# Optimization experiments

Hardware: AMD Instinct MI355X
Metric: run time of the kernel (lower is better)

Reference implementation:

```python
import jax, jax.numpy as jnp
import numpy as np

TIME_SHIFT_START = 256
VELOCITY_START = 768
NOTE_OFF_START = 128
RHYTHM_W = 1.0
HARMONY_W = 1.0
MELODY_W = 1.0


def setup_inputs() -> dict:
    key = jax.random.key(0)
    tokens = jax.random.randint(key, (512, 16384), 0, 774, dtype=jnp.int64)
    return {"tokens": tokens}


def reference(tokens) -> jnp.ndarray:
    batch_size, seq_len = tokens.shape

    # --- rhythm consistency: |diff| of time-shift indicator, mean over all ---
    time_shifts = ((tokens >= TIME_SHIFT_START) & (tokens < VELOCITY_START)).astype(jnp.float32)
    rhythm_loss = jnp.abs(jnp.diff(time_shifts, axis=1)).mean()

    # --- harmonic coherence: vectorized version of the per-position loop ---
    # original: sum_i mean_b(harsh[:, i]) / seq_len  ==  harsh.sum() / (batch * seq_len)
    note_on_mask = tokens < NOTE_OFF_START
    pitches = tokens * note_on_mask.astype(tokens.dtype)
    pitch_classes = pitches % 12                      # [B, S]
    interval = jnp.abs(pitch_classes[:, :-1] - pitch_classes[:, 1:])  # [B, S-1]
    harsh = ((interval == 6) | (interval == 11)).astype(jnp.float32)
    harmony_loss = harsh.sum() / (batch_size * seq_len)

    # --- melodic smoothness: large leap (>12 semitones) rate ---
    pitch_diffs = jnp.diff(pitches.astype(jnp.float32), axis=1)
    melody_loss = (jnp.abs(pitch_diffs) > 12).astype(jnp.float32).mean()

    return RHYTHM_W * rhythm_loss + HARMONY_W * harmony_loss + MELODY_W * melody_loss
```

## Files before the change

### kernel.cpp

```cpp
#include <hip/hip_runtime.h>

constexpr int B = 512;
constexpr int S = 16384;
constexpr int NTOK = B * S;
constexpr int TPT = 32;
constexpr int NBLOCKS = NTOK / TPT / 256;

__global__ __launch_bounds__(256) void mpl_main(const int* __restrict__ tokens,
                                                unsigned int* __restrict__ partials) {
    const int tid = blockIdx.x * 256 + threadIdx.x;
    const int lane = threadIdx.x & 63;
    const int t0 = tid * TPT;

    int toks[TPT + 1];
    const int4* p = reinterpret_cast<const int4*>(tokens + t0);
#pragma unroll
    for (int v = 0; v < TPT / 4; ++v) {
        int4 x = p[v];
        toks[v * 4 + 0] = x.x;
        toks[v * 4 + 1] = x.y;
        toks[v * 4 + 2] = x.z;
        toks[v * 4 + 3] = x.w;
    }

    int nxt = __shfl(toks[0], lane + 1, 64);
    if (lane == 63) {
        const bool rowEnd = ((t0 + TPT) & (S - 1)) == 0;
        nxt = rowEnd ? toks[TPT - 1] : tokens[t0 + TPT];
    }
    toks[TPT] = nxt;

    int rc = 0, hc = 0, mc = 0;
    int qp = 0, pcp = 0, pitp = 0;
#pragma unroll
    for (int j = 0; j <= TPT; ++j) {
        const int t = toks[j];
        const int q = (t + 256) >> 9;
        const int pit = (t < 128) ? t : 0;
        const int pc = pit % 12;
        if (j > 0) {
            rc += (qp ^ q) & 1;
            const int xh = pcp - pc + 11;
            hc += (0x00420021u >> xh) & 1;
            const unsigned ym = (unsigned)(pitp - pit + 12);
            mc += (ym > 24u) ? 1 : 0;
        }
        qp = q; pcp = pc; pitp = pit;
    }

    unsigned int pk = (unsigned)rc | ((unsigned)mc << 16);
    unsigned int hh = (unsigned)hc;
#pragma unroll
    for (int off = 32; off > 0; off >>= 1) {
        pk += __shfl_down(pk, off, 64);
        hh += __shfl_down(hh, off, 64);
    }

    __shared__ unsigned int s[2][4];
    const int wave = threadIdx.x >> 6;
    if ((threadIdx.x & 63) == 0) {
        s[0][wave] = pk;
        s[1][wave] = hh;
    }
    __syncthreads();
    if (threadIdx.x == 0) {
        partials[blockIdx.x]           = s[0][0] + s[0][1] + s[0][2] + s[0][3];
        partials[NBLOCKS + blockIdx.x] = s[1][0] + s[1][1] + s[1][2] + s[1][3];
    }
}

__global__ __launch_bounds__(256) void mpl_reduce(const unsigned int* __restrict__ partials,
                                                  float* __restrict__ out) {
    const uint4* ppk = reinterpret_cast<const uint4*>(partials);
    const uint4* phh = reinterpret_cast<const uint4*>(partials + NBLOCKS);
    unsigned int r = 0, m = 0, h = 0;
#pragma unroll 1
    for (int j = threadIdx.x; j < NBLOCKS / 4; j += 256) {
        uint4 a = ppk[j];
        r += (a.x & 0xFFFFu) + (a.y & 0xFFFFu) + (a.z & 0xFFFFu) + (a.w & 0xFFFFu);
        m += (a.x >> 16) + (a.y >> 16) + (a.z >> 16) + (a.w >> 16);
        uint4 b = phh[j];
        h += b.x + b.y + b.z + b.w;
    }
#pragma unroll
    for (int off = 32; off > 0; off >>= 1) {
        r += __shfl_down(r, off, 64);
        m += __shfl_down(m, off, 64);
        h += __shfl_down(h, off, 64);
    }
    __shared__ unsigned int s[3][4];
    const int wave = threadIdx.x >> 6;
    if ((threadIdx.x & 63) == 0) {
        s[0][wave] = r; s[1][wave] = m; s[2][wave] = h;
    }
    __syncthreads();
    if (threadIdx.x == 0) {
        unsigned int rt = s[0][0] + s[0][1] + s[0][2] + s[0][3];
        unsigned int mt = s[1][0] + s[1][1] + s[1][2] + s[1][3];
        unsigned int ht = s[2][0] + s[2][1] + s[2][2] + s[2][3];
        const double pairs = (double)B * (double)(S - 1);
        const double all = (double)B * (double)S;
        out[0] = (float)((double)rt / pairs + (double)ht / all + (double)mt / pairs);
    }
}

extern "C" void kernel_launch(void* const* d_in, const int* in_sizes, int n_in,
                              void* d_out, int out_size, void* d_ws, size_t ws_size,
                              hipStream_t stream) {
    const int* tokens = (const int*)d_in[0];
    unsigned int* partials = (unsigned int*)d_ws;

    mpl_main<<<NBLOCKS, 256, 0, stream>>>(tokens, partials);
    mpl_reduce<<<1, 256, 0, stream>>>(partials, (float*)d_out);
}
```

Baseline: 15.83 us.

## Fuse final reduction into main kernel via atomics and last-block ticket

Drops the separate reduce kernel launch. Each block atomically adds a packed 64-bit value holding its rhythm, harmony and melody counts into one of 32 cache-line-spaced accumulators, then takes a ticket. The last block sums the accumulators and writes the output. This needs a memset of the workspace before each call, so one launch is replaced by a memset plus atomic traffic, and the 21-bit packed fields rely on carry handling.

```diff
diff --git a/kernel.cpp b/kernel.cpp
--- a/kernel.cpp
+++ b/kernel.cpp
@@ -5,9 +5,12 @@
 constexpr int NTOK = B * S;
 constexpr int TPT = 32;
 constexpr int NBLOCKS = NTOK / TPT / 256;
+constexpr int NLINES = 32;
+constexpr int WS_ZERO_BYTES = NLINES * 64 + 64;
 
-__global__ __launch_bounds__(256) void mpl_main(const int* __restrict__ tokens,
-                                                unsigned int* __restrict__ partials) {
+__global__ __launch_bounds__(256) void mpl_fused(const int* __restrict__ tokens,
+                                                 unsigned long long* __restrict__ ws64,
+                                                 float* __restrict__ out) {
     const int tid = blockIdx.x * 256 + threadIdx.x;
     const int lane = threadIdx.x & 63;
     const int t0 = tid * TPT;
@@ -57,50 +60,50 @@
     }
 
     __shared__ unsigned int s[2][4];
+    __shared__ unsigned int sLast;
     const int wave = threadIdx.x >> 6;
     if ((threadIdx.x & 63) == 0) {
         s[0][wave] = pk;
         s[1][wave] = hh;
     }
     __syncthreads();
+
+    unsigned int* ticket = reinterpret_cast<unsigned int*>(ws64 + NLINES * 8);
+
     if (threadIdx.x == 0) {
-        partials[blockIdx.x]           = s[0][0] + s[0][1] + s[0][2] + s[0][3];
-        partials[NBLOCKS + blockIdx.x] = s[1][0] + s[1][1] + s[1][2] + s[1][3];
-    }
-}
-
-__global__ __launch_bounds__(256) void mpl_reduce(const unsigned int* __restrict__ partials,
-                                                  float* __restrict__ out) {
-    const uint4* ppk = reinterpret_cast<const uint4*>(partials);
-    const uint4* phh = reinterpret_cast<const uint4*>(partials + NBLOCKS);
-    unsigned int r = 0, m = 0, h = 0;
-#pragma unroll 1
-    for (int j = threadIdx.x; j < NBLOCKS / 4; j += 256) {
-        uint4 a = ppk[j];
-        r += (a.x & 0xFFFFu) + (a.y & 0xFFFFu) + (a.z & 0xFFFFu) + (a.w & 0xFFFFu);
-        m += (a.x >> 16) + (a.y >> 16) + (a.z >> 16) + (a.w >> 16);
-        uint4 b = phh[j];
-        h += b.x + b.y + b.z + b.w;
-    }
-#pragma unroll
-    for (int off = 32; off > 0; off >>= 1) {
-        r += __shfl_down(r, off, 64);
-        m += __shfl_down(m, off, 64);
-        h += __shfl_down(h, off, 64);
-    }
-    __shared__ unsigned int s[3][4];
-    const int wave = threadIdx.x >> 6;
-    if ((threadIdx.x & 63) == 0) {
-        s[0][wave] = r; s[1][wave] = m; s[2][wave] = h;
+        const unsigned int pks = s[0][0] + s[0][1] + s[0][2] + s[0][3];
+        const unsigned int hs  = s[1][0] + s[1][1] + s[1][2] + s[1][3];
+        const unsigned long long packed =
+            (unsigned long long)(pks & 0xFFFFu) |
+            ((unsigned long long)hs << 21) |
+            ((unsigned long long)(pks >> 16) << 42);
+        const int line = (blockIdx.x & (NLINES - 1)) * 8;
+        unsigned long long prev = atomicAdd(&ws64[line], packed);
+        unsigned int bump = (unsigned int)(prev >> 63);
+        unsigned int old = atomicAdd(ticket, 1u + bump);
+        sLast = (old == (unsigned)(NBLOCKS - 1)) ? 1u : 0u;
     }
     __syncthreads();
-    if (threadIdx.x == 0) {
-        unsigned int rt = s[0][0] + s[0][1] + s[0][2] + s[0][3];
-        unsigned int mt = s[1][0] + s[1][1] + s[1][2] + s[1][3];
-        unsigned int ht = s[2][0] + s[2][1] + s[2][2] + s[2][3];
-        const double pairs = (double)B * (double)(S - 1);
-        const double all = (double)B * (double)S;
-        out[0] = (float)((double)rt / pairs + (double)ht / all + (double)mt / pairs);
+
+    if (sLast && threadIdx.x < 64) {
+        unsigned int r = 0, h = 0, m = 0;
+        if (threadIdx.x < NLINES) {
+            unsigned long long v = atomicAdd(&ws64[threadIdx.x * 8], 0ull);
+            r = (unsigned int)(v & 0x1FFFFFull);
+            h = (unsigned int)((v >> 21) & 0x1FFFFFull);
+            m = (unsigned int)(v >> 42);
+        }
+#pragma unroll
+        for (int off = 16; off > 0; off >>= 1) {
+            r += __shfl_down(r, off, 64);
+            h += __shfl_down(h, off, 64);
+            m += __shfl_down(m, off, 64);
+        }
+        if (threadIdx.x == 0) {
+            const double pairs = (double)B * (double)(S - 1);
+            const double all = (double)B * (double)S;
+            out[0] = (float)((double)r / pairs + (double)h / all + (double)m / pairs);
+        }
     }
 }
 
@@ -108,8 +111,8 @@
                               void* d_out, int out_size, void* d_ws, size_t ws_size,
                               hipStream_t stream) {
     const int* tokens = (const int*)d_in[0];
-    unsigned int* partials = (unsigned int*)d_ws;
+    unsigned long long* ws64 = (unsigned long long*)d_ws;
 
-    mpl_main<<<NBLOCKS, 256, 0, stream>>>(tokens, partials);
-    mpl_reduce<<<1, 256, 0, stream>>>(partials, (float*)d_out);
+    hipMemsetAsync(d_ws, 0, WS_ZERO_BYTES, stream);
+    mpl_fused<<<NBLOCKS, 256, 0, stream>>>(tokens, ws64, (float*)d_out);
 }
```

After: 27.46 us. +73.5%, slower.
